# Kernel optimization log

Measured on AMD Instinct MI355X. Metric: run time of the kernel, lower is better.

Reference implementation:

```python
import jax, jax.numpy as jnp
import numpy as np

B, N, H, E, L = 64, 100, 128, 128, 3  # batch, nodes, node_hidden, edge_hidden, gcn layers


def setup_inputs() -> dict:
    key = jax.random.key(0)
    ks = jax.random.split(key, 12)
    s = 0.05
    return dict(
        node=jax.random.normal(ks[0], (B, N, 2), jnp.float32),
        demand=jax.random.uniform(ks[1], (B, N), jnp.float32),
        dis=jax.random.uniform(ks[2], (B, N, N), jnp.float32),
        Wn0=jax.random.normal(ks[3], (3, H), jnp.float32) * s,
        bn0=jnp.zeros((H,), jnp.float32),
        Ws=jax.random.normal(ks[4], (L, H, H), jnp.float32) * s,
        Wngh=jax.random.normal(ks[5], (L, H, H), jnp.float32) * s,
        We=jax.random.normal(ks[6], (E,), jnp.float32) * s,
        be=jnp.zeros((E,), jnp.float32),
        Wih=jax.random.normal(ks[7], (2, H, 3 * H), jnp.float32) * s,
        Whh=jax.random.normal(ks[8], (2, H, 3 * H), jnp.float32) * s,
        bih=jnp.zeros((2, 3 * H), jnp.float32),
        bhh=jnp.zeros((2, 3 * H), jnp.float32),
        Wq=jax.random.normal(ks[9], (H, H), jnp.float32) * s,
        Wc=jax.random.normal(ks[10], (E, 2), jnp.float32) * s,
        bc=jnp.zeros((2,), jnp.float32),
    )


def _gru(xin, h, Wih, Whh, bih, bhh):
    gi = xin @ Wih + bih
    gh = h @ Whh + bhh
    ir, iz, inn = jnp.split(gi, 3, -1)
    hr, hz, hn = jnp.split(gh, 3, -1)
    r = jax.nn.sigmoid(ir + hr)
    z = jax.nn.sigmoid(iz + hz)
    n = jnp.tanh(inn + r * hn)
    return (1.0 - z) * n + z * h


def _decode(x, Wih, Whh, bih, bhh, Wq, sample, key):
    b, n, h = x.shape
    scale = 1.0 / np.sqrt(h).astype(np.float32)

    def step(carry, _):
        last, hid, k = carry
        emb = x[jnp.arange(b), last]                      # [b,h]
        h0 = _gru(emb, hid[0], Wih[0], Whh[0], bih[0], bhh[0])
        h1 = _gru(h0, hid[1], Wih[1], Whh[1], bih[1], bhh[1])
        logits = jnp.einsum('bh,bnh->bn', h1 @ Wq, x) * scale
        logp = jax.nn.log_softmax(logits, -1)
        k, sk = jax.random.split(k)
        if sample:
            ind = jax.random.categorical(sk, logits)
        else:
            ind = jnp.argmax(logits, -1)
        ind = ind.astype(jnp.int32)
        chosen = jnp.take_along_axis(logp, ind[:, None], 1)[:, 0]
        return (ind, jnp.stack([h0, h1]), k), (ind, chosen)

    init = (jnp.zeros((b,), jnp.int32), jnp.zeros((2, b, h), x.dtype), key)
    _, (inds, lps) = jax.lax.scan(step, init, None, length=n - 1)
    solution = jnp.concatenate([jnp.zeros((b, 1), jnp.int32), inds.T], axis=1)  # depot 0 first
    return lps.T, solution  # logprob [b,n-1], solution [b,n]


def _count_dist(sol, dis):
    bidx = jnp.arange(sol.shape[0])[:, None]
    return dis[bidx, sol[:, :-1], sol[:, 1:]].sum(axis=1, keepdims=True)  # [b,1]


def reference(node, demand, dis, Wn0, bn0, Ws, Wngh, We, be, Wih, Whh, bih, bhh, Wq, Wc, bc):
    # --- GCN encoder ---
    h = jax.nn.relu(jnp.concatenate([node, demand[..., None]], -1) @ Wn0 + bn0)  # [B,N,H]
    A = jax.nn.softmax(-dis, -1)  # distance-based soft adjacency
    for l in range(Ws.shape[0]):
        h = jax.nn.relu(h @ Ws[l] + jnp.einsum('bij,bjh->bih', A, h @ Wngh[l]))
    e = jax.nn.relu(dis[..., None] * We + be)  # [B,N,N,E]

    key = jax.random.key(42)
    k1, _ = jax.random.split(key)
    sample_logprob, sample_solution = _decode(h, Wih, Whh, bih, bhh, Wq, True, k1)
    sample_distance = _count_dist(sample_solution, dis)
    _, greedy_solution = _decode(h, Wih, Whh, bih, bhh, Wq, False, k1)
    greedy_distance = _count_dist(greedy_solution, dis)

    predict_matrix = jax.nn.softmax(e @ Wc + bc, -1)  # [B,N,N,2]

    b, n = h.shape[0], h.shape[1]
    bidx = jnp.arange(b)[:, None]
    greedy_solution_matrix = (
        jnp.zeros((b, n, n), jnp.int32)
        .at[bidx, greedy_solution[:, :-1], greedy_solution[:, 1:]]
        .set(1)
    )
    return (sample_logprob, sample_distance, greedy_distance, predict_matrix, greedy_solution_matrix)
```

## Files before the change

### kernel.cpp

```cpp
#include <hip/hip_runtime.h>
#include <math.h>

#define BB 64
#define NN 100
#define HH 128
#define T3 384

#define O0 0
#define O1 6336
#define O2 6400
#define O3 6464
#define O4 1286464

#define TINYF 1.17549435e-38f
#define SCALEF 0.08838834764831845f

__device__ __forceinline__ unsigned rotl32(unsigned x, int d) {
    return (x << d) | (x >> (32 - d));
}

__device__ __forceinline__ void tf2x32(unsigned ks0, unsigned ks1,
                                       unsigned x0, unsigned x1,
                                       unsigned& o0, unsigned& o1) {
    unsigned ks2 = ks0 ^ ks1 ^ 0x1BD11BDAu;
    x0 += ks0; x1 += ks1;
    x0 += x1; x1 = rotl32(x1, 13); x1 ^= x0;
    x0 += x1; x1 = rotl32(x1, 15); x1 ^= x0;
    x0 += x1; x1 = rotl32(x1, 26); x1 ^= x0;
    x0 += x1; x1 = rotl32(x1, 6);  x1 ^= x0;
    x0 += ks1; x1 += ks2 + 1u;
    x0 += x1; x1 = rotl32(x1, 17); x1 ^= x0;
    x0 += x1; x1 = rotl32(x1, 29); x1 ^= x0;
    x0 += x1; x1 = rotl32(x1, 16); x1 ^= x0;
    x0 += x1; x1 = rotl32(x1, 24); x1 ^= x0;
    x0 += ks2; x1 += ks0 + 2u;
    x0 += x1; x1 = rotl32(x1, 13); x1 ^= x0;
    x0 += x1; x1 = rotl32(x1, 15); x1 ^= x0;
    x0 += x1; x1 = rotl32(x1, 26); x1 ^= x0;
    x0 += x1; x1 = rotl32(x1, 6);  x1 ^= x0;
    x0 += ks0; x1 += ks1 + 3u;
    x0 += x1; x1 = rotl32(x1, 17); x1 ^= x0;
    x0 += x1; x1 = rotl32(x1, 29); x1 ^= x0;
    x0 += x1; x1 = rotl32(x1, 16); x1 ^= x0;
    x0 += x1; x1 = rotl32(x1, 24); x1 ^= x0;
    x0 += ks1; x1 += ks2 + 4u;
    x0 += x1; x1 = rotl32(x1, 13); x1 ^= x0;
    x0 += x1; x1 = rotl32(x1, 15); x1 ^= x0;
    x0 += x1; x1 = rotl32(x1, 26); x1 ^= x0;
    x0 += x1; x1 = rotl32(x1, 6);  x1 ^= x0;
    x0 += ks2; x1 += ks0 + 5u;
    o0 = x0; o1 = x1;
}

__device__ __forceinline__ float gumbel_f(unsigned k0, unsigned k1, unsigned f) {
    unsigned o0, o1;
    tf2x32(k0, k1, 0u, f, o0, o1);
    unsigned bits = o0 ^ o1;
    float u01 = __uint_as_float((bits >> 9) | 0x3F800000u) - 1.0f;
    float u = fmaxf(TINYF, u01 * (1.0f - TINYF) + TINYF);
    return -logf(-logf(u));
}

__global__ void k_embed_adj(const float* __restrict__ node, const float* __restrict__ demand,
                            const float* __restrict__ Wn0, const float* __restrict__ bn0,
                            const float* __restrict__ dis,
                            float* __restrict__ h, float* __restrict__ A) {
    int bid = blockIdx.x, tid = threadIdx.x;
    if (bid < 3200) {
        int idx = bid * 256 + tid;
        int r = idx >> 7, c = idx & 127;
        float v = node[r * 2] * Wn0[c] + node[r * 2 + 1] * Wn0[128 + c]
                + demand[r] * Wn0[256 + c] + bn0[c];
        h[idx] = fmaxf(v, 0.0f);
    } else {
        int row = (bid - 3200) * 4 + (tid >> 6);
        int l = tid & 63;
        const float* d = dis + row * NN;
        float v0 = -d[l];
        float v1 = (l + 64 < NN) ? -d[l + 64] : -__builtin_inff();
        float m = fmaxf(v0, v1);
        for (int off = 32; off > 0; off >>= 1) m = fmaxf(m, __shfl_xor(m, off));
        float e0 = expf(v0 - m);
        float e1 = (l + 64 < NN) ? expf(v1 - m) : 0.0f;
        float s = e0 + e1;
        for (int off = 32; off > 0; off >>= 1) s += __shfl_xor(s, off);
        float inv = 1.0f / s;
        A[row * NN + l] = e0 * inv;
        if (l + 64 < NN) A[row * NN + l + 64] = e1 * inv;
    }
}

__global__ void k_hw16(const float* __restrict__ h, const float* __restrict__ W,
                       float* __restrict__ out) {
    __shared__ float hs[16 * 128];
    int block_row = blockIdx.x * 16;
    int tid = threadIdx.x;
    int col = tid & 127;
    int rg = tid >> 7;
    for (int i = tid; i < 16 * 128; i += 256) hs[i] = h[block_row * 128 + i];
    __syncthreads();
    float acc[8] = {0.f, 0.f, 0.f, 0.f, 0.f, 0.f, 0.f, 0.f};
    for (int k = 0; k < 128; k++) {
        float w = W[k * 128 + col];
#pragma unroll
        for (int r = 0; r < 8; r++) acc[r] += hs[(rg + 2 * r) * 128 + k] * w;
    }
#pragma unroll
    for (int r = 0; r < 8; r++)
        out[(block_row + rg + 2 * r) * 128 + col] = acc[r];
}

__global__ void k_zp(const float* __restrict__ h, const float* __restrict__ WqT,
                     const float* __restrict__ Wih, const float* __restrict__ bih,
                     float* __restrict__ Z, float* __restrict__ P0) {
    __shared__ float hs[16 * 128];
    int block_row = blockIdx.x * 16;
    int tid = threadIdx.x;
    int c = tid & 127;
    int rg = tid >> 7;
    int y = blockIdx.y;
    for (int i = tid; i < 16 * 128; i += 256) hs[i] = h[block_row * 128 + i];
    __syncthreads();
    float acc[8] = {0.f, 0.f, 0.f, 0.f, 0.f, 0.f, 0.f, 0.f};
    if (y == 0) {
        for (int k = 0; k < 128; k++) {
            float w = WqT[k * 128 + c];
#pragma unroll
            for (int r = 0; r < 8; r++) acc[r] += hs[(rg + 2 * r) * 128 + k] * w;
        }
#pragma unroll
        for (int r = 0; r < 8; r++)
            Z[(block_row + rg + 2 * r) * 128 + c] = acc[r];
    } else {
        int col = (y - 1) * 128 + c;
        for (int k = 0; k < 128; k++) {
            float w = Wih[k * 384 + col];
#pragma unroll
            for (int r = 0; r < 8; r++) acc[r] += hs[(rg + 2 * r) * 128 + k] * w;
        }
        float bb = bih[col];
#pragma unroll
        for (int r = 0; r < 8; r++)
            P0[(size_t)(block_row + rg + 2 * r) * 384 + col] = acc[r] + bb;
    }
}

__global__ void k_transpose128(const float* __restrict__ Wq, float* __restrict__ WqT) {
    int i = blockIdx.x * 256 + threadIdx.x;
    if (i >= 128 * 128) return;
    int k = i >> 7, c = i & 127;
    WqT[k * 128 + c] = Wq[c * 128 + k];
}

__global__ void k_agg10(const float* __restrict__ h, const float* __restrict__ Ws,
                        const float* __restrict__ A, const float* __restrict__ hw,
                        float* __restrict__ out) {
    __shared__ float hs[10 * 128];
    __shared__ float As[10 * 100];
    int b = blockIdx.x / 10;
    int i0 = (blockIdx.x % 10) * 10;
    int tid = threadIdx.x;
    int col = tid & 127;
    int rg = tid >> 7;
    int rowbase = b * NN + i0;
    for (int i = tid; i < 10 * 128; i += 256) hs[i] = h[rowbase * 128 + i];
    for (int i = tid; i < 10 * 100; i += 256) As[i] = A[rowbase * 100 + i];
    __syncthreads();
    float acc[5] = {0.f, 0.f, 0.f, 0.f, 0.f};
    for (int k = 0; k < 128; k++) {
        float w = Ws[k * 128 + col];
#pragma unroll
        for (int r = 0; r < 5; r++) acc[r] += hs[(rg + 2 * r) * 128 + k] * w;
    }
    const float* hwb = hw + b * NN * 128;
    for (int j = 0; j < NN; j++) {
        float v = hwb[j * 128 + col];
#pragma unroll
        for (int r = 0; r < 5; r++) acc[r] += As[(rg + 2 * r) * 100 + j] * v;
    }
#pragma unroll
    for (int r = 0; r < 5; r++)
        out[(rowbase + rg + 2 * r) * 128 + col] = fmaxf(acc[r], 0.0f);
}

__global__ void k_predict_zero(const float* __restrict__ dis, const float* __restrict__ We,
                               const float* __restrict__ be, const float* __restrict__ Wc,
                               const float* __restrict__ bc, float* __restrict__ out3,
                               float* __restrict__ zp) {
    int bid = blockIdx.x, tid = threadIdx.x;
    if (bid >= 1250) {
        int i = (bid - 1250) * 256 + tid;
        float4 z; z.x = 0.f; z.y = 0.f; z.z = 0.f; z.w = 0.f;
        ((float4*)zp)[i] = z;
        return;
    }
    __shared__ float sWe[128], sbe[128], sc0[128], sc1[128];
    if (tid < 128) {
        sWe[tid] = We[tid];
        sbe[tid] = be[tid];
        sc0[tid] = Wc[tid * 2];
        sc1[tid] = Wc[tid * 2 + 1];
    }
    __syncthreads();
    float b0 = bc[0], b1 = bc[1];
    int p0 = bid * 512 + tid, p1 = p0 + 256;
    float d0 = dis[p0], d1 = dis[p1];
    float a00 = b0, a01 = b1, a10 = b0, a11 = b1;
    for (int k = 0; k < 128; k++) {
        float we = sWe[k], bbe = sbe[k], c0 = sc0[k], c1 = sc1[k];
        float e0 = fmaxf(d0 * we + bbe, 0.0f);
        float e1 = fmaxf(d1 * we + bbe, 0.0f);
        a00 += e0 * c0; a01 += e0 * c1;
        a10 += e1 * c0; a11 += e1 * c1;
    }
    {
        float m = fmaxf(a00, a01);
        float q0 = expf(a00 - m), q1 = expf(a01 - m);
        float inv = 1.0f / (q0 + q1);
        out3[p0 * 2] = q0 * inv;
        out3[p0 * 2 + 1] = q1 * inv;
    }
    {
        float m = fmaxf(a10, a11);
        float q0 = expf(a10 - m), q1 = expf(a11 - m);
        float inv = 1.0f / (q0 + q1);
        out3[p1 * 2] = q0 * inv;
        out3[p1 * 2 + 1] = q1 * inv;
    }
}

__device__ __forceinline__ void matvec_tile4(const float* __restrict__ W,
                                             const float* __restrict__ hp,
                                             int nk4,
                                             float* __restrict__ pg0,
                                             float* __restrict__ pg1) {
    float a00 = 0.f, a01 = 0.f, a02 = 0.f, a03 = 0.f;
    float a10 = 0.f, a11 = 0.f, a12 = 0.f, a13 = 0.f;
#pragma unroll 4
    for (int k4 = 0; k4 < nk4; ++k4) {
        float4 hA = *(const float4*)(hp + 4 * k4);
        float4 hB = *(const float4*)(hp + 132 + 4 * k4);
        const float* Wk = W + (size_t)(4 * k4) * T3;
        float4 w0 = *(const float4*)(Wk);
        float4 w1 = *(const float4*)(Wk + T3);
        float4 w2 = *(const float4*)(Wk + 2 * T3);
        float4 w3 = *(const float4*)(Wk + 3 * T3);
        a00 += hA.x * w0.x; a01 += hA.x * w0.y; a02 += hA.x * w0.z; a03 += hA.x * w0.w;
        a10 += hB.x * w0.x; a11 += hB.x * w0.y; a12 += hB.x * w0.z; a13 += hB.x * w0.w;
        a00 += hA.y * w1.x; a01 += hA.y * w1.y; a02 += hA.y * w1.z; a03 += hA.y * w1.w;
        a10 += hB.y * w1.x; a11 += hB.y * w1.y; a12 += hB.y * w1.z; a13 += hB.y * w1.w;
        a00 += hA.z * w2.x; a01 += hA.z * w2.y; a02 += hA.z * w2.z; a03 += hA.z * w2.w;
        a10 += hB.z * w2.x; a11 += hB.z * w2.y; a12 += hB.z * w2.z; a13 += hB.z * w2.w;
        a00 += hA.w * w3.x; a01 += hA.w * w3.y; a02 += hA.w * w3.z; a03 += hA.w * w3.w;
        a10 += hB.w * w3.x; a11 += hB.w * w3.y; a12 += hB.w * w3.z; a13 += hB.w * w3.w;
    }
    float4 o;
    o.x = a00; o.y = a01; o.z = a02; o.w = a03;
    *(float4*)pg0 = o;
    o.x = a10; o.y = a11; o.z = a12; o.w = a13;
    *(float4*)pg1 = o;
}

__global__ __launch_bounds__(512, 2) void k_decode4(
    const float* __restrict__ P0, const float* __restrict__ Z,
    const float* __restrict__ dis,
    const float* __restrict__ Wih, const float* __restrict__ Whh,
    const float* __restrict__ bih, const float* __restrict__ bhh,
    float* __restrict__ out) {
    __shared__ float Zs[NN * 132];
    __shared__ float h0s[2 * 132], h1s[2 * 132];
    __shared__ float gi0s[2 * 384];
    __shared__ float pgA[2 * 2 * 392];
    __shared__ float pgB[2 * 2 * 392];
    __shared__ float pgC[4 * 2 * 392];
    __shared__ float sbhh0[T3], sbih1[T3], sbhh1[T3];
    __shared__ float pl[2 * 2 * 100];
    __shared__ float gum[128];
    __shared__ int s_ind2[2];

    const int tid = threadIdx.x;
    const int b = blockIdx.x;
    const float* __restrict__ Wih1 = Wih + 128 * T3;

    for (int i4 = tid; i4 < NN * 32; i4 += 512) {
        int r = i4 >> 5, c4 = (i4 & 31) * 4;
        *(float4*)&Zs[r * 132 + c4] = *(const float4*)&Z[(b * NN + r) * 128 + c4];
    }
    if (tid < T3) {
        sbhh0[tid] = bhh[tid];
        sbih1[tid] = bih[T3 + tid];
        sbhh1[tid] = bhh[T3 + tid];
    }
    if (tid < 256) {
        int m = tid >> 7, i = tid & 127;
        h0s[m * 132 + i] = 0.0f;
        h1s[m * 132 + i] = 0.0f;
    }
    if (tid == 0) { s_ind2[0] = 0; s_ind2[1] = 0; }

    unsigned kk0, kk1;
    tf2x32(0u, 42u, 0u, 0u, kk0, kk1);

    int lastm = 0;
    float dist = 0.0f;
    __syncthreads();

    for (int t = 0; t < NN - 1; t++) {
        if (tid < 384) {
            const int unit = tid / 192;
            const int r = tid - unit * 192;
            const int ks = r / 96, j4 = r - ks * 96;
            const int j0 = j4 * 4, k0 = ks * 64;
            const float* W = Whh + unit * (128 * T3) + (size_t)k0 * T3 + j0;
            const float* hp = ((unit == 0) ? h0s : h1s) + k0;
            float* pg = (unit == 0) ? pgA : pgB;
            matvec_tile4(W, hp, 16,
                         &pg[(ks * 2 + 0) * 392 + j0],
                         &pg[(ks * 2 + 1) * 392 + j0]);
        } else {
            int u = tid - 384;
            int l0 = s_ind2[0], l1 = s_ind2[1];
#pragma unroll
            for (int q = 0; q < 6; q++) {
                int f = u + 128 * q;
                int m = (f >= 384) ? 1 : 0;
                int j = f - m * 384;
                gi0s[f] = P0[(size_t)(b * NN + (m ? l1 : l0)) * T3 + j];
            }
            unsigned sk0, sk1, nk0, nk1;
            tf2x32(kk0, kk1, 0u, 1u, sk0, sk1);
            tf2x32(kk0, kk1, 0u, 0u, nk0, nk1);
            kk0 = nk0; kk1 = nk1;
            if (u < NN) gum[u] = gumbel_f(sk0, sk1, (unsigned)(b * NN + u));
        }
        __syncthreads();

        if (tid < 256) {
            int m = tid >> 7, i = tid & 127;
            float ghr = pgA[(0 * 2 + m) * 392 + i]       + pgA[(1 * 2 + m) * 392 + i]       + sbhh0[i];
            float ghz = pgA[(0 * 2 + m) * 392 + i + 128] + pgA[(1 * 2 + m) * 392 + i + 128] + sbhh0[i + 128];
            float ghn = pgA[(0 * 2 + m) * 392 + i + 256] + pgA[(1 * 2 + m) * 392 + i + 256] + sbhh0[i + 256];
            float rr = 1.0f / (1.0f + expf(-(gi0s[m * 384 + i] + ghr)));
            float zz = 1.0f / (1.0f + expf(-(gi0s[m * 384 + i + 128] + ghz)));
            float nn = tanhf(gi0s[m * 384 + i + 256] + rr * ghn);
            h0s[m * 132 + i] = (1.0f - zz) * nn + zz * h0s[m * 132 + i];
        }
        __syncthreads();

        if (tid < 384) {
            const int ks = tid / 96, j4 = tid - ks * 96;
            const int j0 = j4 * 4, k0 = ks * 32;
            const float* W = Wih1 + (size_t)k0 * T3 + j0;
            matvec_tile4(W, h0s + k0, 8,
                         &pgC[(ks * 2 + 0) * 392 + j0],
                         &pgC[(ks * 2 + 1) * 392 + j0]);
        }
        __syncthreads();

        if (tid < 256) {
            int m = tid >> 7, i = tid & 127;
            float gir = sbih1[i], giz = sbih1[i + 128], gin = sbih1[i + 256];
#pragma unroll
            for (int ks = 0; ks < 4; ks++) {
                int pb = (ks * 2 + m) * 392;
                gir += pgC[pb + i];
                giz += pgC[pb + i + 128];
                gin += pgC[pb + i + 256];
            }
            float ghr = pgB[(0 * 2 + m) * 392 + i]       + pgB[(1 * 2 + m) * 392 + i]       + sbhh1[i];
            float ghz = pgB[(0 * 2 + m) * 392 + i + 128] + pgB[(1 * 2 + m) * 392 + i + 128] + sbhh1[i + 128];
            float ghn = pgB[(0 * 2 + m) * 392 + i + 256] + pgB[(1 * 2 + m) * 392 + i + 256] + sbhh1[i + 256];
            float rr = 1.0f / (1.0f + expf(-(gir + ghr)));
            float zz = 1.0f / (1.0f + expf(-(giz + ghz)));
            float nn = tanhf(gin + rr * ghn);
            h1s[m * 132 + i] = (1.0f - zz) * nn + zz * h1s[m * 132 + i];
        }
        __syncthreads();

        if (tid < 200) {
            int ks = tid / 100, n = tid - ks * 100;
            int kk0p = ks * 64;
            const float* Zp = &Zs[n * 132 + kk0p];
            const float* hp = &h1s[kk0p];
            float a0 = 0.f, a1 = 0.f;
#pragma unroll 4
            for (int q = 0; q < 16; q++) {
                float4 z4 = *(const float4*)(Zp + 4 * q);
                float4 hA = *(const float4*)(hp + 4 * q);
                float4 hB = *(const float4*)(hp + 132 + 4 * q);
                a0 += hA.x * z4.x; a0 += hA.y * z4.y; a0 += hA.z * z4.z; a0 += hA.w * z4.w;
                a1 += hB.x * z4.x; a1 += hB.y * z4.y; a1 += hB.z * z4.z; a1 += hB.w * z4.w;
            }
            pl[(0 * 2 + ks) * 100 + n] = a0;
            pl[(1 * 2 + ks) * 100 + n] = a1;
        }
        __syncthreads();

        if (tid < 128) {
            const int m = tid >> 6, lane = tid & 63;
            float v0, v1 = -__builtin_inff();
            v0 = (pl[(m * 2 + 0) * 100 + lane] + pl[(m * 2 + 1) * 100 + lane]) * SCALEF;
            if (lane + 64 < NN)
                v1 = (pl[(m * 2 + 0) * 100 + lane + 64] + pl[(m * 2 + 1) * 100 + lane + 64]) * SCALEF;
            float mx = fmaxf(v0, v1);
            for (int off = 32; off > 0; off >>= 1) mx = fmaxf(mx, __shfl_xor(mx, off));
            float e = expf(v0 - mx) + ((lane + 64 < NN) ? expf(v1 - mx) : 0.0f);
            for (int off = 32; off > 0; off >>= 1) e += __shfl_xor(e, off);
            float a0 = v0, a1 = v1;
            if (m == 0) {
                a0 += gum[lane];
                if (lane + 64 < NN) a1 += gum[lane + 64];
            }
            float bv; int bi;
            if (a1 > a0) { bv = a1; bi = lane + 64; } else { bv = a0; bi = lane; }
            for (int off = 32; off > 0; off >>= 1) {
                float ov = __shfl_xor(bv, off);
                int   oi = __shfl_xor(bi, off);
                if (ov > bv || (ov == bv && oi < bi)) { bv = ov; bi = oi; }
            }
            int ind = bi;
            float la = __shfl(v0, ind & 63);
            float lb = __shfl(v1, ind & 63);
            float lv = (ind < 64) ? la : lb;
            if (lane == 0) {
                if (m == 0) out[O0 + b * (NN - 1) + t] = lv - mx - logf(e);
                else        out[O4 + (size_t)b * NN * NN + lastm * NN + ind] = 1.0f;
                s_ind2[m] = ind;
            }
            dist += dis[b * NN * NN + lastm * NN + ind];
            lastm = ind;
        }
        __syncthreads();
    }

    if (tid == 0)  out[O1 + b] = dist;
    if (tid == 64) out[O2 + b] = dist;
}

extern "C" void kernel_launch(void* const* d_in, const int* in_sizes, int n_in,
                              void* d_out, int out_size, void* d_ws, size_t ws_size,
                              hipStream_t stream) {
    (void)in_sizes; (void)n_in; (void)out_size; (void)ws_size;
    const float* node   = (const float*)d_in[0];
    const float* demand = (const float*)d_in[1];
    const float* dis    = (const float*)d_in[2];
    const float* Wn0    = (const float*)d_in[3];
    const float* bn0    = (const float*)d_in[4];
    const float* Ws     = (const float*)d_in[5];
    const float* Wngh   = (const float*)d_in[6];
    const float* We     = (const float*)d_in[7];
    const float* be     = (const float*)d_in[8];
    const float* Wih    = (const float*)d_in[9];
    const float* Whh    = (const float*)d_in[10];
    const float* bih    = (const float*)d_in[11];
    const float* bhh    = (const float*)d_in[12];
    const float* Wq     = (const float*)d_in[13];
    const float* Wc     = (const float*)d_in[14];
    const float* bc     = (const float*)d_in[15];
    float* out = (float*)d_out;
    float* ws  = (float*)d_ws;

    float* hA  = ws;
    float* hB  = ws + 819200;
    float* hw  = ws + 1638400;
    float* A   = ws + 2457600;
    float* P0  = ws + 2457600;
    float* WqT = ws + 4915200;

    hipLaunchKernelGGL(k_predict_zero, dim3(1875), dim3(256), 0, stream,
                       dis, We, be, Wc, bc, out + O3, out + O4);

    hipLaunchKernelGGL(k_embed_adj, dim3(4800), dim3(256), 0, stream,
                       node, demand, Wn0, bn0, dis, hA, A);

    float* cur = hA;
    float* nxt = hB;
    for (int l = 0; l < 3; l++) {
        hipLaunchKernelGGL(k_hw16, dim3(400), dim3(256), 0, stream, cur, Wngh + l * 16384, hw);
        hipLaunchKernelGGL(k_agg10, dim3(640), dim3(256), 0, stream, cur, Ws + l * 16384, A, hw, nxt);
        float* tswap = cur; cur = nxt; nxt = tswap;
    }

    hipLaunchKernelGGL(k_transpose128, dim3(64), dim3(256), 0, stream, Wq, WqT);
    hipLaunchKernelGGL(k_zp, dim3(400, 4), dim3(256), 0, stream, cur, WqT, Wih, bih, hw, P0);

    hipLaunchKernelGGL(k_decode4, dim3(64), dim3(512), 0, stream,
                       P0, hw, dis, Wih, Whh, bih, bhh, out);
}
```

Measured before the change: 979.6 us.

## Widen decode kernel to 768 threads with finer K-split matvecs

The sequential decode kernel grows from 512 to 768 threads per block. The Whh and Wih1 matvecs are split over more K-slices (4 and 8 partial sums) so each thread runs a shorter loop. The P0 gather now goes straight into registers of the GRU threads instead of through a shared staging buffer, and the Gumbel noise is computed alongside the first GRU update. This shortens the latency-bound per-step critical path, at the cost of more partial-sum reduction work and more register pressure from the higher launch bound.

New measurement: 923.4 us. 1.06x faster.

```diff
diff --git a/kernel.cpp b/kernel.cpp
--- a/kernel.cpp
+++ b/kernel.cpp
@@ -261,18 +261,20 @@
     *(float4*)pg1 = o;
 }
 
-__global__ __launch_bounds__(512, 2) void k_decode4(
-    const float* __restrict__ P0, const float* __restrict__ Z,
+__global__ __launch_bounds__(768, 3) void k_decode9(
+    const float* __restrict__ P0,
+    const float* __restrict__ Z,
     const float* __restrict__ dis,
-    const float* __restrict__ Wih, const float* __restrict__ Whh,
-    const float* __restrict__ bih, const float* __restrict__ bhh,
+    const float* __restrict__ Wih,
+    const float* __restrict__ Whh,
+    const float* __restrict__ bih,
+    const float* __restrict__ bhh,
     float* __restrict__ out) {
     __shared__ float Zs[NN * 132];
     __shared__ float h0s[2 * 132], h1s[2 * 132];
-    __shared__ float gi0s[2 * 384];
-    __shared__ float pgA[2 * 2 * 392];
-    __shared__ float pgB[2 * 2 * 392];
-    __shared__ float pgC[4 * 2 * 392];
+    __shared__ float pgA[4 * 2 * 392];
+    __shared__ float pgB[4 * 2 * 392];
+    __shared__ float pgC[8 * 2 * 392];
     __shared__ float sbhh0[T3], sbih1[T3], sbhh1[T3];
     __shared__ float pl[2 * 2 * 100];
     __shared__ float gum[128];
@@ -280,9 +282,10 @@
 
     const int tid = threadIdx.x;
     const int b = blockIdx.x;
+
     const float* __restrict__ Wih1 = Wih + 128 * T3;
 
-    for (int i4 = tid; i4 < NN * 32; i4 += 512) {
+    for (int i4 = tid; i4 < NN * 32; i4 += 768) {
         int r = i4 >> 5, c4 = (i4 & 31) * 4;
         *(float4*)&Zs[r * 132 + c4] = *(const float4*)&Z[(b * NN + r) * 128 + c4];
     }
@@ -301,59 +304,67 @@
     unsigned kk0, kk1;
     tf2x32(0u, 42u, 0u, 0u, kk0, kk1);
 
+    const int unitA = tid / 384;
+    const int rA = tid - unitA * 384;
+    const int ksA = rA / 96, j4A = rA - ksA * 96;
+    const int j0A = j4A * 4, k0A = ksA * 32;
+    const int ksC = tid / 96, j4C = tid - ksC * 96;
+    const int j0C = j4C * 4, k0C = ksC * 16;
+
     int lastm = 0;
     float dist = 0.0f;
     __syncthreads();
 
     for (int t = 0; t < NN - 1; t++) {
-        if (tid < 384) {
-            const int unit = tid / 192;
-            const int r = tid - unit * 192;
-            const int ks = r / 96, j4 = r - ks * 96;
-            const int j0 = j4 * 4, k0 = ks * 64;
-            const float* W = Whh + unit * (128 * T3) + (size_t)k0 * T3 + j0;
-            const float* hp = ((unit == 0) ? h0s : h1s) + k0;
-            float* pg = (unit == 0) ? pgA : pgB;
-            matvec_tile4(W, hp, 16,
-                         &pg[(ks * 2 + 0) * 392 + j0],
-                         &pg[(ks * 2 + 1) * 392 + j0]);
-        } else {
-            int u = tid - 384;
-            int l0 = s_ind2[0], l1 = s_ind2[1];
-#pragma unroll
-            for (int q = 0; q < 6; q++) {
-                int f = u + 128 * q;
-                int m = (f >= 384) ? 1 : 0;
-                int j = f - m * 384;
-                gi0s[f] = P0[(size_t)(b * NN + (m ? l1 : l0)) * T3 + j];
-            }
-            unsigned sk0, sk1, nk0, nk1;
-            tf2x32(kk0, kk1, 0u, 1u, sk0, sk1);
-            tf2x32(kk0, kk1, 0u, 0u, nk0, nk1);
-            kk0 = nk0; kk1 = nk1;
-            if (u < NN) gum[u] = gumbel_f(sk0, sk1, (unsigned)(b * NN + u));
+        unsigned sk0, sk1, nkA, nkB;
+        tf2x32(kk0, kk1, 0u, 1u, sk0, sk1);
+        tf2x32(kk0, kk1, 0u, 0u, nkA, nkB);
+        kk0 = nkA; kk1 = nkB;
+
+        float pf_r = 0.f, pf_z = 0.f, pf_n = 0.f;
+        if (tid < 256) {
+            const float* P0row = P0 + (size_t)(b * NN + s_ind2[tid >> 7]) * T3;
+            int i = tid & 127;
+            pf_r = P0row[i];
+            pf_z = P0row[i + 128];
+            pf_n = P0row[i + 256];
+        }
+
+        {
+            const float* W = Whh + unitA * (128 * T3) + (size_t)k0A * T3 + j0A;
+            const float* hp = ((unitA == 0) ? h0s : h1s) + k0A;
+            float* pg = (unitA == 0) ? pgA : pgB;
+            matvec_tile4(W, hp, 8,
+                         &pg[(ksA * 2 + 0) * 392 + j0A],
+                         &pg[(ksA * 2 + 1) * 392 + j0A]);
         }
         __syncthreads();
 
         if (tid < 256) {
             int m = tid >> 7, i = tid & 127;
-            float ghr = pgA[(0 * 2 + m) * 392 + i]       + pgA[(1 * 2 + m) * 392 + i]       + sbhh0[i];
-            float ghz = pgA[(0 * 2 + m) * 392 + i + 128] + pgA[(1 * 2 + m) * 392 + i + 128] + sbhh0[i + 128];
-            float ghn = pgA[(0 * 2 + m) * 392 + i + 256] + pgA[(1 * 2 + m) * 392 + i + 256] + sbhh0[i + 256];
-            float rr = 1.0f / (1.0f + expf(-(gi0s[m * 384 + i] + ghr)));
-            float zz = 1.0f / (1.0f + expf(-(gi0s[m * 384 + i + 128] + ghz)));
-            float nn = tanhf(gi0s[m * 384 + i + 256] + rr * ghn);
+            float ghr = sbhh0[i], ghz = sbhh0[i + 128], ghn = sbhh0[i + 256];
+#pragma unroll
+            for (int ks = 0; ks < 4; ks++) {
+                int pb = (ks * 2 + m) * 392;
+                ghr += pgA[pb + i];
+                ghz += pgA[pb + i + 128];
+                ghn += pgA[pb + i + 256];
+            }
+            float rr = 1.0f / (1.0f + expf(-(pf_r + ghr)));
+            float zz = 1.0f / (1.0f + expf(-(pf_z + ghz)));
+            float nn = tanhf(pf_n + rr * ghn);
             h0s[m * 132 + i] = (1.0f - zz) * nn + zz * h0s[m * 132 + i];
+        } else if (tid < 356) {
+            int u = tid - 256;
+            gum[u] = gumbel_f(sk0, sk1, (unsigned)(b * NN + u));
         }
         __syncthreads();
 
-        if (tid < 384) {
-            const int ks = tid / 96, j4 = tid - ks * 96;
-            const int j0 = j4 * 4, k0 = ks * 32;
-            const float* W = Wih1 + (size_t)k0 * T3 + j0;
-            matvec_tile4(W, h0s + k0, 8,
-                         &pgC[(ks * 2 + 0) * 392 + j0],
-                         &pgC[(ks * 2 + 1) * 392 + j0]);
+        {
+            const float* W = Wih1 + (size_t)k0C * T3 + j0C;
+            matvec_tile4(W, h0s + k0C, 4,
+                         &pgC[(ksC * 2 + 0) * 392 + j0C],
+                         &pgC[(ksC * 2 + 1) * 392 + j0C]);
         }
         __syncthreads();
 
@@ -361,15 +372,20 @@
             int m = tid >> 7, i = tid & 127;
             float gir = sbih1[i], giz = sbih1[i + 128], gin = sbih1[i + 256];
 #pragma unroll
-            for (int ks = 0; ks < 4; ks++) {
+            for (int ks = 0; ks < 8; ks++) {
                 int pb = (ks * 2 + m) * 392;
                 gir += pgC[pb + i];
                 giz += pgC[pb + i + 128];
                 gin += pgC[pb + i + 256];
             }
-            float ghr = pgB[(0 * 2 + m) * 392 + i]       + pgB[(1 * 2 + m) * 392 + i]       + sbhh1[i];
-            float ghz = pgB[(0 * 2 + m) * 392 + i + 128] + pgB[(1 * 2 + m) * 392 + i + 128] + sbhh1[i + 128];
-            float ghn = pgB[(0 * 2 + m) * 392 + i + 256] + pgB[(1 * 2 + m) * 392 + i + 256] + sbhh1[i + 256];
+            float ghr = sbhh1[i], ghz = sbhh1[i + 128], ghn = sbhh1[i + 256];
+#pragma unroll
+            for (int ks = 0; ks < 4; ks++) {
+                int pb = (ks * 2 + m) * 392;
+                ghr += pgB[pb + i];
+                ghz += pgB[pb + i + 128];
+                ghn += pgB[pb + i + 256];
+            }
             float rr = 1.0f / (1.0f + expf(-(gir + ghr)));
             float zz = 1.0f / (1.0f + expf(-(giz + ghz)));
             float nn = tanhf(gin + rr * ghn);
@@ -484,6 +500,6 @@
     hipLaunchKernelGGL(k_transpose128, dim3(64), dim3(256), 0, stream, Wq, WqT);
     hipLaunchKernelGGL(k_zp, dim3(400, 4), dim3(256), 0, stream, cur, WqT, Wih, bih, hw, P0);
 
-    hipLaunchKernelGGL(k_decode4, dim3(64), dim3(512), 0, stream,
+    hipLaunchKernelGGL(k_decode9, dim3(64), dim3(768), 0, stream,
                        P0, hw, dis, Wih, Whh, bih, bhh, out);
 }
```
